# Kernel tuning notes

Hardware: AMD Instinct MI355X
Metric: run time of the kernel (lower is better)

The kernel has to match this reference:

```python
import jax, jax.numpy as jnp
import numpy as np

N = 50000  # num nodes

def gcn_conv(x, edge_index, W, b, num_nodes):
    # x: [N, Fin] -> [N, Fout]; PyG GCNConv: linear, add self-loops, sym-norm aggregate, bias
    h = x @ W
    row, col = edge_index[0], edge_index[1]  # source j, target i
    loop = jnp.arange(num_nodes, dtype=row.dtype)
    row = jnp.concatenate([row, loop])
    col = jnp.concatenate([col, loop])
    deg = jax.ops.segment_sum(jnp.ones_like(col, dtype=h.dtype), col, num_segments=num_nodes)
    dinv = jnp.where(deg > 0, jax.lax.rsqrt(deg), 0.0)
    norm = dinv[row] * dinv[col]                      # [E+N]
    msg = h[row] * norm[:, None]                      # gather + scale
    out = jax.ops.segment_sum(msg, col, num_segments=num_nodes)
    return out + b

def setup_inputs() -> dict:
    key = jax.random.key(0)
    ks = jax.random.split(key, 8)
    F_in, H1, H2 = 128, 128, 64
    E_train, E_score = 600000, 200000
    x = jax.random.normal(ks[0], (N, F_in), dtype=jnp.float32)
    train_pos_edge_index = jax.random.randint(ks[1], (2, E_train), 0, N, dtype=jnp.int32)
    pos_edge_index = jax.random.randint(ks[2], (2, E_score), 0, N, dtype=jnp.int32)
    neg_edge_index = jax.random.randint(ks[3], (2, E_score), 0, N, dtype=jnp.int32)
    W1 = jax.random.normal(ks[4], (F_in, H1), dtype=jnp.float32) / np.sqrt(F_in)
    b1 = jnp.zeros((H1,), dtype=jnp.float32)
    W2 = jax.random.normal(ks[5], (H1, H2), dtype=jnp.float32) / np.sqrt(H1)
    b2 = jnp.zeros((H2,), dtype=jnp.float32)
    return {"x": x, "train_pos_edge_index": train_pos_edge_index,
            "pos_edge_index": pos_edge_index, "neg_edge_index": neg_edge_index,
            "W1": W1, "b1": b1, "W2": W2, "b2": b2}

def reference(x, train_pos_edge_index, pos_edge_index, neg_edge_index, W1, b1, W2, b2):
    h = jax.nn.relu(gcn_conv(x, train_pos_edge_index, W1, b1, N))
    h = gcn_conv(h, train_pos_edge_index, W2, b2, N)
    total = jnp.concatenate([pos_edge_index, neg_edge_index], axis=-1)  # [2, Ep+En]
    x_j = h[total[0]]
    x_i = h[total[1]]
    return jnp.einsum('ef,ef->e', x_i, x_j)
```

## Files before the change

kernel.cpp:

```cpp
#include <hip/hip_runtime.h>
#include <hip/hip_bf16.h>
#include <hip/hip_fp16.h>

#define NODES   50000
#define E_TRAIN 600000
#define E_SCORE 200000
#define CAP     48
#define G1B     782
#define CHUNK   2048
#define BINB    294
#define NB_C    391
#define SCAP    48
#define WTB     32

typedef unsigned short ushort_t;
typedef __attribute__((ext_vector_type(8))) short bf16x8;
typedef __attribute__((ext_vector_type(4))) float f32x4;

static __device__ __forceinline__ float bf2f(unsigned short u) {
    return __uint_as_float((unsigned int)u << 16);
}
static __device__ __forceinline__ unsigned short f2bf(float f) {
    __hip_bfloat16 h = __float2bfloat16(f);
    return *reinterpret_cast<unsigned short*>(&h);
}
static __device__ __forceinline__ unsigned short f2h(float f) {
    __half h = __float2half(f);
    return *reinterpret_cast<unsigned short*>(&h);
}
static __device__ __forceinline__ float2 u2f2(unsigned int u) {
    __half2 h = *reinterpret_cast<__half2*>(&u);
    return __half22float2(h);
}
static __device__ __forceinline__ unsigned int f22u(float a, float b) {
    __half2 h = __floats2half2_rn(a, b);
    return *reinterpret_cast<unsigned int*>(&h);
}
static __device__ __forceinline__ unsigned int f22u_bf(float a, float b) {
    return (unsigned int)f2bf(a) | ((unsigned int)f2bf(b) << 16);
}
static __device__ __forceinline__ bf16x8 cvt8(const float* p) {
    float4 v0 = *(const float4*)p;
    float4 v1 = *(const float4*)(p + 4);
    bf16x8 r;
    r[0] = (short)f2bf(v0.x); r[1] = (short)f2bf(v0.y);
    r[2] = (short)f2bf(v0.z); r[3] = (short)f2bf(v0.w);
    r[4] = (short)f2bf(v1.x); r[5] = (short)f2bf(v1.y);
    r[6] = (short)f2bf(v1.z); r[7] = (short)f2bf(v1.w);
    return r;
}

__global__ __launch_bounds__(256) void k13_bin_gemm1_w(
    const int* __restrict__ trow, const int* __restrict__ tcol,
    unsigned int* __restrict__ cbuf2, int* __restrict__ hcntT,
    const unsigned int* __restrict__ xw,
    const void* __restrict__ x, const void* __restrict__ W1,
    const void* __restrict__ b1, const void* __restrict__ W2,
    const void* __restrict__ b2,
    ushort_t* __restrict__ W2T, float* __restrict__ b1f, float* __restrict__ b2f,
    int* __restrict__ flag, ushort_t* __restrict__ g1)
{
    __shared__ __align__(16) int smi[8708];
    const int b = blockIdx.x, t = threadIdx.x;

    if (b < BINB) {
        int* cur = smi;
        for (int i = t; i < 512; i += 256) cur[i] = 0;
        __syncthreads();
        unsigned int* my = cbuf2 + (size_t)b * (NB_C * SCAP);
        #pragma unroll
        for (int k = 0; k < 8; ++k) {
            int e = b * CHUNK + k * 256 + t;
            if (e < E_TRAIN) {
                unsigned int d = (unsigned int)tcol[e];
                unsigned int s = (unsigned int)trow[e];
                int bk = (int)(d >> 7);
                int slot = atomicAdd(&cur[bk], 1);
                if (slot < SCAP)
                    my[bk * SCAP + slot] = (d << 16) | s;
            }
        }
        __syncthreads();
        for (int i = t; i < NB_C; i += 256) hcntT[i * BINB + b] = cur[i];
        return;
    }

    int* cvp = &smi[8704];
    if (t == 0) *cvp = 0;
    __syncthreads();
    {
        unsigned int wv = xw[t];
        int ex = ((wv & 0xFFFFu) >> 7) & 0xFF;
        if (ex >= 100 && ex <= 140) atomicAdd(cvp, 1);
    }
    __syncthreads();
    const bool isbf = *cvp >= 150;

    if (b < BINB + G1B) {
        ushort_t* wlds = (ushort_t*)smi;
        for (int idx = t; idx < 16384; idx += 256) {
            int k = idx >> 7, n = idx & 127;
            int pos = n * 136 + ((((k >> 3) ^ (n & 7)) << 3) | (k & 7));
            wlds[pos] = isbf ? ((const ushort_t*)W1)[idx] : f2bf(((const float*)W1)[idx]);
        }
        __syncthreads();

        const int bb = b - BINB;
        const int lane = t & 63, wave = t >> 6;
        const int n = lane & 15, quad = lane >> 4;
        const int wr0 = bb * 64 + wave * 16;
        int rowA = wr0 + n; if (rowA > NODES - 1) rowA = NODES - 1;
        f32x4 acc[8];
        #pragma unroll
        for (int ct = 0; ct < 8; ++ct) acc[ct] = (f32x4){0.f, 0.f, 0.f, 0.f};
        #pragma unroll
        for (int kc = 0; kc < 4; ++kc) {
            bf16x8 a;
            if (isbf) a = *(const bf16x8*)((const ushort_t*)x + (long)rowA * 128 + kc * 32 + quad * 8);
            else      a = cvt8((const float*)x + (long)rowA * 128 + kc * 32 + quad * 8);
            #pragma unroll
            for (int ct = 0; ct < 8; ++ct) {
                int row = ct * 16 + n;
                int chk = ((kc << 2) | quad) ^ (n & 7);
                bf16x8 bv = *(const bf16x8*)&wlds[row * 136 + (chk << 3)];
                acc[ct] = __builtin_amdgcn_mfma_f32_16x16x32_bf16(a, bv, acc[ct], 0, 0, 0);
            }
        }
        #pragma unroll
        for (int ct = 0; ct < 8; ++ct)
            #pragma unroll
            for (int r = 0; r < 4; ++r) {
                int orow = wr0 + quad * 4 + r;
                if (orow < NODES)
                    g1[(long)orow * 128 + ct * 16 + n] = f2h(acc[ct][r]);
            }
        return;
    }

    const int bw = b - BINB - G1B;
    if (bw == 0 && t == 0) flag[0] = isbf ? 1 : 0;
    int tid = bw * 256 + t;
    {
        int k = tid >> 6, n = tid & 63;
        W2T[n * 128 + k] = isbf ? ((const ushort_t*)W2)[tid] : f2bf(((const float*)W2)[tid]);
    }
    if (tid < 128) b1f[tid] = isbf ? bf2f(((const ushort_t*)b1)[tid]) : ((const float*)b1)[tid];
    if (tid < 64)  b2f[tid] = isbf ? bf2f(((const ushort_t*)b2)[tid]) : ((const float*)b2)[tid];
}

__global__ __launch_bounds__(256) void k2_fine(
    const unsigned int* __restrict__ cbuf2, const int* __restrict__ hcntT,
    int* __restrict__ esrc, int* __restrict__ cnt, float* __restrict__ dinvA)
{
    __shared__ int lcnt[128];
    __shared__ __align__(16) int lists[128 * CAP];
    const int bk = blockIdx.x, t = threadIdx.x;
    for (int i = t; i < 128; i += 256) lcnt[i] = 0;
    __syncthreads();
    const int st0 = t >> 1, sub = t & 1;
    for (int s0 = st0; s0 < BINB; s0 += 128) {
        int c = hcntT[bk * BINB + s0];
        if (c > SCAP) c = SCAP;
        const unsigned int* src = cbuf2 + ((size_t)s0 * NB_C + bk) * SCAP;
        for (int j = sub; j < c; j += 2) {
            unsigned int p = src[j];
            int fd = (int)((p >> 16) & 127);
            int s  = (int)(p & 0xFFFFu);
            int slot = atomicAdd(&lcnt[fd], 1);
            if (slot < CAP) lists[fd * CAP + slot] = s;
        }
    }
    __syncthreads();
    if (t < 128) {
        int d = bk * 128 + t;
        if (d < NODES) {
            int c = lcnt[t];
            cnt[d] = c;
            dinvA[d] = rsqrtf((float)c + 1.0f);
        }
    }
    const uint4* lv = (const uint4*)lists;
    uint4* ev = (uint4*)esrc;
    for (int i = t; i < 128 * CAP / 4; i += 256)
        ev[(long)bk * (128 * CAP / 4) + i] = lv[i];
}

__global__ __launch_bounds__(256) void k4_gather1_gemm2(
    const ushort_t* __restrict__ g1, const int* __restrict__ cnt,
    const float* __restrict__ dinvA,
    const int* __restrict__ esrc, const float* __restrict__ b1f,
    const ushort_t* __restrict__ W2T, ushort_t* __restrict__ g2)
{
    __shared__ ushort_t h1S[16 * 136];
    const int t = threadIdx.x;
    const int lane = t & 63, wave = t >> 6;
    const int quarter = lane >> 4, ql = lane & 15;
    const int d0 = blockIdx.x * 16;
    const int r = wave * 4 + quarter;
    const int d = d0 + r;
    const uint4* g1v = (const uint4*)g1;

    const int cdeg = cnt[d];
    const int m = cdeg < CAP ? cdeg : CAP;
    const int base = d * CAP;
    float a0=0.f,a1=0.f,a2=0.f,a3=0.f,a4=0.f,a5=0.f,a6=0.f,a7=0.f;
    int j = 0;
    for (; j + 4 <= m; j += 4) {
        int4 s4 = *(const int4*)&esrc[base + j];
        float ds0 = dinvA[s4.x], ds1 = dinvA[s4.y], ds2 = dinvA[s4.z], ds3 = dinvA[s4.w];
        uint4 v0 = g1v[(long)s4.x * 16 + ql];
        uint4 v1 = g1v[(long)s4.y * 16 + ql];
        uint4 v2 = g1v[(long)s4.z * 16 + ql];
        uint4 v3 = g1v[(long)s4.w * 16 + ql];
        float2 p;
        p = u2f2(v0.x); a0 = fmaf(p.x, ds0, a0); a1 = fmaf(p.y, ds0, a1);
        p = u2f2(v0.y); a2 = fmaf(p.x, ds0, a2); a3 = fmaf(p.y, ds0, a3);
        p = u2f2(v0.z); a4 = fmaf(p.x, ds0, a4); a5 = fmaf(p.y, ds0, a5);
        p = u2f2(v0.w); a6 = fmaf(p.x, ds0, a6); a7 = fmaf(p.y, ds0, a7);
        p = u2f2(v1.x); a0 = fmaf(p.x, ds1, a0); a1 = fmaf(p.y, ds1, a1);
        p = u2f2(v1.y); a2 = fmaf(p.x, ds1, a2); a3 = fmaf(p.y, ds1, a3);
        p = u2f2(v1.z); a4 = fmaf(p.x, ds1, a4); a5 = fmaf(p.y, ds1, a5);
        p = u2f2(v1.w); a6 = fmaf(p.x, ds1, a6); a7 = fmaf(p.y, ds1, a7);
        p = u2f2(v2.x); a0 = fmaf(p.x, ds2, a0); a1 = fmaf(p.y, ds2, a1);
        p = u2f2(v2.y); a2 = fmaf(p.x, ds2, a2); a3 = fmaf(p.y, ds2, a3);
        p = u2f2(v2.z); a4 = fmaf(p.x, ds2, a4); a5 = fmaf(p.y, ds2, a5);
        p = u2f2(v2.w); a6 = fmaf(p.x, ds2, a6); a7 = fmaf(p.y, ds2, a7);
        p = u2f2(v3.x); a0 = fmaf(p.x, ds3, a0); a1 = fmaf(p.y, ds3, a1);
        p = u2f2(v3.y); a2 = fmaf(p.x, ds3, a2); a3 = fmaf(p.y, ds3, a3);
        p = u2f2(v3.z); a4 = fmaf(p.x, ds3, a4); a5 = fmaf(p.y, ds3, a5);
        p = u2f2(v3.w); a6 = fmaf(p.x, ds3, a6); a7 = fmaf(p.y, ds3, a7);
    }
    for (; j < m; ++j) {
        int s0 = esrc[base + j];
        float ds0 = dinvA[s0];
        uint4 v0 = g1v[(long)s0 * 16 + ql];
        float2 p;
        p = u2f2(v0.x); a0 = fmaf(p.x, ds0, a0); a1 = fmaf(p.y, ds0, a1);
        p = u2f2(v0.y); a2 = fmaf(p.x, ds0, a2); a3 = fmaf(p.y, ds0, a3);
        p = u2f2(v0.z); a4 = fmaf(p.x, ds0, a4); a5 = fmaf(p.y, ds0, a5);
        p = u2f2(v0.w); a6 = fmaf(p.x, ds0, a6); a7 = fmaf(p.y, ds0, a7);
    }
    float dd = dinvA[d];
    uint4 gv = g1v[(long)d * 16 + ql];
    float4 bA = *(const float4*)(b1f + ql * 8);
    float4 bB = *(const float4*)(b1f + ql * 8 + 4);
    float2 p;
    p = u2f2(gv.x); float w0 = fmaxf(dd * (a0 + dd * p.x) + bA.x, 0.f), w1 = fmaxf(dd * (a1 + dd * p.y) + bA.y, 0.f);
    p = u2f2(gv.y); float w2 = fmaxf(dd * (a2 + dd * p.x) + bA.z, 0.f), w3 = fmaxf(dd * (a3 + dd * p.y) + bA.w, 0.f);
    p = u2f2(gv.z); float w4 = fmaxf(dd * (a4 + dd * p.x) + bB.x, 0.f), w5 = fmaxf(dd * (a5 + dd * p.y) + bB.y, 0.f);
    p = u2f2(gv.w); float w6 = fmaxf(dd * (a6 + dd * p.x) + bB.z, 0.f), w7 = fmaxf(dd * (a7 + dd * p.y) + bB.w, 0.f);
    {
        uint4 ov;
        ov.x = f22u_bf(w0, w1); ov.y = f22u_bf(w2, w3);
        ov.z = f22u_bf(w4, w5); ov.w = f22u_bf(w6, w7);
        *(uint4*)&h1S[r * 136 + ql * 8] = ov;
    }
    __syncthreads();

    const int n = lane & 15, quad = lane >> 4;
    f32x4 acc = (f32x4){0.f, 0.f, 0.f, 0.f};
    #pragma unroll
    for (int kc = 0; kc < 4; ++kc) {
        bf16x8 a = *(const bf16x8*)&h1S[n * 136 + kc * 32 + quad * 8];
        bf16x8 bv = *(const bf16x8*)(W2T + (wave * 16 + n) * 128 + kc * 32 + quad * 8);
        acc = __builtin_amdgcn_mfma_f32_16x16x32_bf16(a, bv, acc, 0, 0, 0);
    }
    __syncthreads();
    #pragma unroll
    for (int rr = 0; rr < 4; ++rr) {
        int drow = quad * 4 + rr;
        float sc = dinvA[d0 + drow];
        h1S[drow * 72 + wave * 16 + n] = f2h(acc[rr] * sc);
    }
    __syncthreads();
    if (t < 128) {
        int row = t >> 3, cir = t & 7;
        *(uint4*)&g2[((long)d0 + row) * 64 + cir * 8] = *(const uint4*)&h1S[row * 72 + cir * 8];
    }
}

__global__ __launch_bounds__(256) void k5_gather2(
    const ushort_t* __restrict__ g2, const int* __restrict__ cnt,
    const float* __restrict__ dinvA,
    const int* __restrict__ esrc, const float* __restrict__ b2f,
    unsigned int* __restrict__ h2)
{
    const int t = threadIdx.x;
    const int lane = t & 63, wave = t >> 6;
    const int oct = lane >> 3, ol = lane & 7;
    const int d = blockIdx.x * 32 + wave * 8 + oct;
    if (d >= NODES) return;
    const uint4* g2v = (const uint4*)g2;

    const int cdeg = cnt[d];
    const int m = cdeg < CAP ? cdeg : CAP;
    const int base = d * CAP;
    float a0=0.f,a1=0.f,a2=0.f,a3=0.f,a4=0.f,a5=0.f,a6=0.f,a7=0.f;
    int j = 0;
    for (; j + 4 <= m; j += 4) {
        int4 s4 = *(const int4*)&esrc[base + j];
        uint4 v0 = g2v[(long)s4.x * 8 + ol];
        uint4 v1 = g2v[(long)s4.y * 8 + ol];
        uint4 v2 = g2v[(long)s4.z * 8 + ol];
        uint4 v3 = g2v[(long)s4.w * 8 + ol];
        float2 p;
        p = u2f2(v0.x); a0 += p.x; a1 += p.y;
        p = u2f2(v0.y); a2 += p.x; a3 += p.y;
        p = u2f2(v0.z); a4 += p.x; a5 += p.y;
        p = u2f2(v0.w); a6 += p.x; a7 += p.y;
        p = u2f2(v1.x); a0 += p.x; a1 += p.y;
        p = u2f2(v1.y); a2 += p.x; a3 += p.y;
        p = u2f2(v1.z); a4 += p.x; a5 += p.y;
        p = u2f2(v1.w); a6 += p.x; a7 += p.y;
        p = u2f2(v2.x); a0 += p.x; a1 += p.y;
        p = u2f2(v2.y); a2 += p.x; a3 += p.y;
        p = u2f2(v2.z); a4 += p.x; a5 += p.y;
        p = u2f2(v2.w); a6 += p.x; a7 += p.y;
        p = u2f2(v3.x); a0 += p.x; a1 += p.y;
        p = u2f2(v3.y); a2 += p.x; a3 += p.y;
        p = u2f2(v3.z); a4 += p.x; a5 += p.y;
        p = u2f2(v3.w); a6 += p.x; a7 += p.y;
    }
    for (; j < m; ++j) {
        uint4 v0 = g2v[(long)esrc[base + j] * 8 + ol];
        float2 p;
        p = u2f2(v0.x); a0 += p.x; a1 += p.y;
        p = u2f2(v0.y); a2 += p.x; a3 += p.y;
        p = u2f2(v0.z); a4 += p.x; a5 += p.y;
        p = u2f2(v0.w); a6 += p.x; a7 += p.y;
    }
    float dd = dinvA[d];
    uint4 gv = g2v[(long)d * 8 + ol];
    float4 bA = *(const float4*)(b2f + ol * 8);
    float4 bB = *(const float4*)(b2f + ol * 8 + 4);
    float2 p0 = u2f2(gv.x), p1 = u2f2(gv.y), p2 = u2f2(gv.z), p3 = u2f2(gv.w);
    uint4 ov;
    ov.x = f22u(dd * (a0 + p0.x) + bA.x, dd * (a1 + p0.y) + bA.y);
    ov.y = f22u(dd * (a2 + p1.x) + bA.z, dd * (a3 + p1.y) + bA.w);
    ov.z = f22u(dd * (a4 + p2.x) + bB.x, dd * (a5 + p2.y) + bB.y);
    ov.w = f22u(dd * (a6 + p3.x) + bB.z, dd * (a7 + p3.y) + bB.w);
    *(uint4*)&h2[(long)d * 32 + ol * 4] = ov;
}

__global__ __launch_bounds__(256) void k6_score(
    const int* __restrict__ pos, const int* __restrict__ neg,
    const unsigned int* __restrict__ h2, void* __restrict__ out,
    const int* __restrict__ flag)
{
    int e = blockIdx.x * 256 + threadIdx.x;
    if (e >= 2 * E_SCORE) return;
    int s, d;
    if (e < E_SCORE) { s = pos[e];           d = pos[E_SCORE + e]; }
    else             { int i = e - E_SCORE; s = neg[i]; d = neg[E_SCORE + i]; }
    const uint4* A = (const uint4*)(h2 + (long)s * 32);
    const uint4* B = (const uint4*)(h2 + (long)d * 32);
    float acc = 0.f;
    #pragma unroll
    for (int q = 0; q < 8; ++q) {
        uint4 ua = A[q], ub = B[q];
        float2 a0 = u2f2(ua.x), b0 = u2f2(ub.x);
        float2 a1 = u2f2(ua.y), b1 = u2f2(ub.y);
        float2 a2 = u2f2(ua.z), b2 = u2f2(ub.z);
        float2 a3 = u2f2(ua.w), b3 = u2f2(ub.w);
        acc += a0.x * b0.x + a0.y * b0.y + a1.x * b1.x + a1.y * b1.y
             + a2.x * b2.x + a2.y * b2.y + a3.x * b3.x + a3.y * b3.y;
    }
    if (flag[0]) ((ushort_t*)out)[e] = f2bf(acc);
    else         ((float*)out)[e] = acc;
}

extern "C" void kernel_launch(void* const* d_in, const int* in_sizes, int n_in,
                              void* d_out, int out_size, void* d_ws, size_t ws_size,
                              hipStream_t stream) {
    const void* x      = d_in[0];
    const int*  etrain = (const int*)d_in[1];
    const int*  pos    = (const int*)d_in[2];
    const int*  neg    = (const int*)d_in[3];
    const void* W1     = d_in[4];
    const void* b1     = d_in[5];
    const void* W2     = d_in[6];
    const void* b2     = d_in[7];

    char* ws = (char*)d_ws;
    int*          flag   = (int*)(ws + 0);
    int*          cnt    = (int*)(ws + 256);
    float*        dinvA  = (float*)(ws + 200448);
    ushort_t*     W2T    = (ushort_t*)(ws + 400640);
    float*        b1f    = (float*)(ws + 417024);
    float*        b2f    = (float*)(ws + 417536);
    int*          hcntT  = (int*)(ws + 417792);
    int*          esrc   = (int*)(ws + 877824);
    unsigned int* cbuf2  = (unsigned int*)(ws + 10487040);
    ushort_t*     g1     = (ushort_t*)(ws + 32558208);
    ushort_t*     g2     = (ushort_t*)(ws + 45358208);
    unsigned int* h2     = (unsigned int*)(ws + 51758208);

    const int* trow = etrain;
    const int* tcol = etrain + E_TRAIN;

    k13_bin_gemm1_w<<<BINB + G1B + WTB, 256, 0, stream>>>(
        trow, tcol, cbuf2, hcntT, (const unsigned int*)x,
        x, W1, b1, W2, b2, W2T, b1f, b2f, flag, g1);

    k2_fine<<<NB_C, 256, 0, stream>>>(cbuf2, hcntT, esrc, cnt, dinvA);

    k4_gather1_gemm2<<<3125, 256, 0, stream>>>(g1, cnt, dinvA, esrc, b1f, W2T, g2);

    k5_gather2<<<1563, 256, 0, stream>>>(g2, cnt, dinvA, esrc, b2f, h2);

    k6_score<<<1563, 256, 0, stream>>>(pos, neg, h2, d_out, flag);
}
```

Before: 187.2 us.

## Split GEMM1 out of binning kernel and pre-transpose W1 to global

Binning and the first GEMM no longer share one fused launch. W1 is now transposed and converted to bf16 once by the weight-prep blocks in the binning kernel. A separate GEMM1 kernel then reads W1T straight from global memory (through cache) instead of staging a swizzled copy in LDS for each block. This removes the per-block LDS staging and lets the binning blocks run with a small shared footprint, but it adds a kernel launch and serialises GEMM1 after binning. B-operand loads also go from LDS to global/L2.

Measured after the change: 183.3 us. 2.1% less time.

```diff
diff --git a/kernel.cpp b/kernel.cpp
--- a/kernel.cpp
+++ b/kernel.cpp
@@ -11,7 +11,7 @@
 #define BINB    294
 #define NB_C    391
 #define SCAP    48
-#define WTB     32
+#define WTB     64
 
 typedef unsigned short ushort_t;
 typedef __attribute__((ext_vector_type(8))) short bf16x8;
@@ -50,21 +50,19 @@
     return r;
 }
 
-__global__ __launch_bounds__(256) void k13_bin_gemm1_w(
+__global__ __launch_bounds__(256) void k1_bin_w(
     const int* __restrict__ trow, const int* __restrict__ tcol,
     unsigned int* __restrict__ cbuf2, int* __restrict__ hcntT,
     const unsigned int* __restrict__ xw,
-    const void* __restrict__ x, const void* __restrict__ W1,
-    const void* __restrict__ b1, const void* __restrict__ W2,
-    const void* __restrict__ b2,
-    ushort_t* __restrict__ W2T, float* __restrict__ b1f, float* __restrict__ b2f,
-    int* __restrict__ flag, ushort_t* __restrict__ g1)
-{
-    __shared__ __align__(16) int smi[8708];
+    const void* __restrict__ W1, const void* __restrict__ b1,
+    const void* __restrict__ W2, const void* __restrict__ b2,
+    ushort_t* __restrict__ W1T, ushort_t* __restrict__ W2T,
+    float* __restrict__ b1f, float* __restrict__ b2f, int* __restrict__ flag)
+{
+    __shared__ int cur[512];
     const int b = blockIdx.x, t = threadIdx.x;
 
     if (b < BINB) {
-        int* cur = smi;
         for (int i = t; i < 512; i += 256) cur[i] = 0;
         __syncthreads();
         unsigned int* my = cbuf2 + (size_t)b * (NB_C * SCAP);
@@ -85,67 +83,64 @@
         return;
     }
 
-    int* cvp = &smi[8704];
-    if (t == 0) *cvp = 0;
+    __shared__ int cv;
+    if (t == 0) cv = 0;
     __syncthreads();
     {
         unsigned int wv = xw[t];
         int ex = ((wv & 0xFFFFu) >> 7) & 0xFF;
-        if (ex >= 100 && ex <= 140) atomicAdd(cvp, 1);
-    }
-    __syncthreads();
-    const bool isbf = *cvp >= 150;
-
-    if (b < BINB + G1B) {
-        ushort_t* wlds = (ushort_t*)smi;
-        for (int idx = t; idx < 16384; idx += 256) {
-            int k = idx >> 7, n = idx & 127;
-            int pos = n * 136 + ((((k >> 3) ^ (n & 7)) << 3) | (k & 7));
-            wlds[pos] = isbf ? ((const ushort_t*)W1)[idx] : f2bf(((const float*)W1)[idx]);
-        }
-        __syncthreads();
-
-        const int bb = b - BINB;
-        const int lane = t & 63, wave = t >> 6;
-        const int n = lane & 15, quad = lane >> 4;
-        const int wr0 = bb * 64 + wave * 16;
-        int rowA = wr0 + n; if (rowA > NODES - 1) rowA = NODES - 1;
-        f32x4 acc[8];
-        #pragma unroll
-        for (int ct = 0; ct < 8; ++ct) acc[ct] = (f32x4){0.f, 0.f, 0.f, 0.f};
-        #pragma unroll
-        for (int kc = 0; kc < 4; ++kc) {
-            bf16x8 a;
-            if (isbf) a = *(const bf16x8*)((const ushort_t*)x + (long)rowA * 128 + kc * 32 + quad * 8);
-            else      a = cvt8((const float*)x + (long)rowA * 128 + kc * 32 + quad * 8);
-            #pragma unroll
-            for (int ct = 0; ct < 8; ++ct) {
-                int row = ct * 16 + n;
-                int chk = ((kc << 2) | quad) ^ (n & 7);
-                bf16x8 bv = *(const bf16x8*)&wlds[row * 136 + (chk << 3)];
-                acc[ct] = __builtin_amdgcn_mfma_f32_16x16x32_bf16(a, bv, acc[ct], 0, 0, 0);
-            }
-        }
-        #pragma unroll
-        for (int ct = 0; ct < 8; ++ct)
-            #pragma unroll
-            for (int r = 0; r < 4; ++r) {
-                int orow = wr0 + quad * 4 + r;
-                if (orow < NODES)
-                    g1[(long)orow * 128 + ct * 16 + n] = f2h(acc[ct][r]);
-            }
-        return;
-    }
-
-    const int bw = b - BINB - G1B;
+        if (ex >= 100 && ex <= 140) atomicAdd(&cv, 1);
+    }
+    __syncthreads();
+    const bool isbf = cv >= 150;
+    const int bw = b - BINB;
     if (bw == 0 && t == 0) flag[0] = isbf ? 1 : 0;
     int tid = bw * 256 + t;
     {
+        int k = tid >> 7, n = tid & 127;
+        W1T[n * 128 + k] = isbf ? ((const ushort_t*)W1)[tid] : f2bf(((const float*)W1)[tid]);
+    }
+    if (tid < 128 * 64) {
         int k = tid >> 6, n = tid & 63;
         W2T[n * 128 + k] = isbf ? ((const ushort_t*)W2)[tid] : f2bf(((const float*)W2)[tid]);
     }
     if (tid < 128) b1f[tid] = isbf ? bf2f(((const ushort_t*)b1)[tid]) : ((const float*)b1)[tid];
     if (tid < 64)  b2f[tid] = isbf ? bf2f(((const ushort_t*)b2)[tid]) : ((const float*)b2)[tid];
+}
+
+__global__ __launch_bounds__(256) void k_gemm1(
+    const void* __restrict__ x, const ushort_t* __restrict__ W1T,
+    ushort_t* __restrict__ g1, const int* __restrict__ flag)
+{
+    const int t = threadIdx.x;
+    const int bb = blockIdx.x;
+    const bool isbf = flag[0] != 0;
+    const int lane = t & 63, wave = t >> 6;
+    const int n = lane & 15, quad = lane >> 4;
+    const int wr0 = bb * 64 + wave * 16;
+    int rowA = wr0 + n; if (rowA > NODES - 1) rowA = NODES - 1;
+    f32x4 acc[8];
+    #pragma unroll
+    for (int ct = 0; ct < 8; ++ct) acc[ct] = (f32x4){0.f, 0.f, 0.f, 0.f};
+    #pragma unroll
+    for (int kc = 0; kc < 4; ++kc) {
+        bf16x8 a;
+        if (isbf) a = *(const bf16x8*)((const ushort_t*)x + (long)rowA * 128 + kc * 32 + quad * 8);
+        else      a = cvt8((const float*)x + (long)rowA * 128 + kc * 32 + quad * 8);
+        #pragma unroll
+        for (int ct = 0; ct < 8; ++ct) {
+            bf16x8 bv = *(const bf16x8*)(W1T + (ct * 16 + n) * 128 + kc * 32 + quad * 8);
+            acc[ct] = __builtin_amdgcn_mfma_f32_16x16x32_bf16(a, bv, acc[ct], 0, 0, 0);
+        }
+    }
+    #pragma unroll
+    for (int ct = 0; ct < 8; ++ct)
+        #pragma unroll
+        for (int r = 0; r < 4; ++r) {
+            int orow = wr0 + quad * 4 + r;
+            if (orow < NODES)
+                g1[(long)orow * 128 + ct * 16 + n] = f2h(acc[ct][r]);
+        }
 }
 
 __global__ __launch_bounds__(256) void k2_fine(
@@ -385,22 +380,25 @@
     int*          flag   = (int*)(ws + 0);
     int*          cnt    = (int*)(ws + 256);
     float*        dinvA  = (float*)(ws + 200448);
-    ushort_t*     W2T    = (ushort_t*)(ws + 400640);
-    float*        b1f    = (float*)(ws + 417024);
-    float*        b2f    = (float*)(ws + 417536);
-    int*          hcntT  = (int*)(ws + 417792);
-    int*          esrc   = (int*)(ws + 877824);
-    unsigned int* cbuf2  = (unsigned int*)(ws + 10487040);
-    ushort_t*     g1     = (ushort_t*)(ws + 32558208);
-    ushort_t*     g2     = (ushort_t*)(ws + 45358208);
-    unsigned int* h2     = (unsigned int*)(ws + 51758208);
+    ushort_t*     W1T    = (ushort_t*)(ws + 400640);
+    ushort_t*     W2T    = (ushort_t*)(ws + 433408);
+    float*        b1f    = (float*)(ws + 449792);
+    float*        b2f    = (float*)(ws + 450304);
+    int*          hcntT  = (int*)(ws + 450560);
+    int*          esrc   = (int*)(ws + 910592);
+    unsigned int* cbuf2  = (unsigned int*)(ws + 10519808);
+    ushort_t*     g1     = (ushort_t*)(ws + 32590976);
+    ushort_t*     g2     = (ushort_t*)(ws + 45403264);
+    unsigned int* h2     = (unsigned int*)(ws + 51809408);
 
     const int* trow = etrain;
     const int* tcol = etrain + E_TRAIN;
 
-    k13_bin_gemm1_w<<<BINB + G1B + WTB, 256, 0, stream>>>(
+    k1_bin_w<<<BINB + WTB, 256, 0, stream>>>(
         trow, tcol, cbuf2, hcntT, (const unsigned int*)x,
-        x, W1, b1, W2, b2, W2T, b1f, b2f, flag, g1);
+        W1, b1, W2, b2, W1T, W2T, b1f, b2f, flag);
+
+    k_gemm1<<<G1B, 256, 0, stream>>>(x, W1T, g1, flag);
 
     k2_fine<<<NB_C, 256, 0, stream>>>(cbuf2, hcntT, esrc, cnt, dinvA);
 
```
